# Optimization experiments

Hardware: AMD Instinct MI355X
Metric: run time of the kernel (lower is better)

## Reference

```python
import jax, jax.numpy as jnp
import numpy as np

WIN = 7


def rel_index(win: int) -> jnp.ndarray:
    ys, xs = jnp.meshgrid(jnp.arange(win), jnp.arange(win), indexing='ij')
    coords = jnp.stack([ys.reshape(-1), xs.reshape(-1)], axis=-1)  # (S, 2)
    diff = coords[None, :, :] - coords[:, None, :] + (win - 1)     # (S, S, 2)
    return diff[..., 0] * (2 * win - 1) + diff[..., 1]             # (S, S)


def setup_inputs() -> dict:
    key = jax.random.key(0)
    ks = jax.random.split(key, 5)
    B, WN, S, C, H = 64, 64, WIN * WIN, 192, 6
    X = jax.random.normal(ks[0], (B, WN, S, C), dtype=jnp.float32)
    # torch nn.Linear(emb_dim, 3*emb_dim) -> store as (in, out) for x @ W
    Wqkv = jax.random.normal(ks[1], (C, 3 * C), dtype=jnp.float32) * 0.02
    bqkv = jnp.zeros((3 * C,), dtype=jnp.float32)
    Wo = jax.random.normal(ks[2], (C, C), dtype=jnp.float32) * 0.02
    bo = jnp.zeros((C,), dtype=jnp.float32)
    bias_table = jax.random.normal(ks[3], ((2 * WIN - 1) ** 2, H), dtype=jnp.float32) * 0.02
    return {"X": X, "Wqkv": Wqkv, "bqkv": bqkv, "Wo": Wo, "bo": bo, "bias_table": bias_table}


def reference(X, Wqkv, bqkv, Wo, bo, bias_table):
    B, WN, S, C = X.shape
    H = bias_table.shape[1]
    D = C // H
    scale = D ** -0.5
    # qkv projection: (B, WN, S, 3C) -> (3, B, WN, H, S, D)
    qkv = (X @ Wqkv + bqkv).reshape(B, WN, S, 3, H, D).transpose(3, 0, 1, 4, 2, 5)
    q, k, v = qkv[0], qkv[1], qkv[2]
    attn = jnp.einsum('bwhqd,bwhkd->bwhqk', q, k) * scale  # (B, WN, H, S, S)
    # gathered relative position bias: (S, S, H) -> (H, S, S)
    idx = rel_index(WIN)
    bias = bias_table[idx].transpose(2, 0, 1)
    attn = attn + bias[None, None]
    proba = jax.nn.softmax(attn, axis=-1)  # dropout omitted (eval mode)
    out = jnp.einsum('bwhqk,bwhkd->bwhqd', proba, v)  # (B, WN, H, S, D)
    out = out.transpose(0, 1, 3, 2, 4).reshape(B, WN, S, C)
    return out @ Wo + bo
```

## Files before the change

kernel.cpp:

```cpp
#include <hip/hip_runtime.h>
#include <hip/hip_bf16.h>


typedef __attribute__((ext_vector_type(4))) float f32x4;
typedef __attribute__((ext_vector_type(8))) short bf16x8;
typedef __attribute__((ext_vector_type(4))) unsigned short u16x4;

#define SCALE 0.17677669529663689f
#define MFMA(a, b, acc) __builtin_amdgcn_mfma_f32_16x16x32_bf16(a, b, acc, 0, 0, 0)

__device__ __forceinline__ unsigned short f2bf(float f) {
  union { float f; unsigned int u; } v; v.f = f;
  return (unsigned short)((v.u + 0x7FFFu + ((v.u >> 16) & 1u)) >> 16);
}

__global__ void wprep(const float* __restrict__ Wqkv, const float* __restrict__ Wo,
                      unsigned short* __restrict__ WqkvT, unsigned short* __restrict__ WoT) {
  int i = blockIdx.x * 256 + threadIdx.x;
  if (i < 576 * 192) { int n = i / 192, k = i % 192; WqkvT[i] = f2bf(Wqkv[k * 576 + n]); }
  if (i < 192 * 192) { int n = i / 192, k = i % 192; WoT[i]   = f2bf(Wo[k * 192 + n]); }
}

__global__ __launch_bounds__(512, 4)
void qkv_gemm(const float* __restrict__ X, const unsigned short* __restrict__ WqkvT,
              const float* __restrict__ bqkv, unsigned short* __restrict__ qkv) {
  __shared__ __align__(16) unsigned short Bs[2][64 * 200];
  __shared__ __align__(16) unsigned short scr[8][16 * 72];

  const int tid = threadIdx.x, w8 = tid >> 6, lane = tid & 63;
  const int g = lane >> 4, c = lane & 15;
  const size_t bm = (size_t)blockIdx.x * 128;
  const f32x4 z = {0.f, 0.f, 0.f, 0.f};

  bf16x8 af[6];
  {
    const float* xr = X + (bm + w8 * 16 + c) * 192;
    #pragma unroll
    for (int ks = 0; ks < 6; ++ks) {
      f32x4 lo = *(const f32x4*)(xr + ks * 32 + g * 8);
      f32x4 hi = *(const f32x4*)(xr + ks * 32 + g * 8 + 4);
      bf16x8 a;
      a[0] = (short)f2bf(lo[0]); a[1] = (short)f2bf(lo[1]);
      a[2] = (short)f2bf(lo[2]); a[3] = (short)f2bf(lo[3]);
      a[4] = (short)f2bf(hi[0]); a[5] = (short)f2bf(hi[1]);
      a[6] = (short)f2bf(hi[2]); a[7] = (short)f2bf(hi[3]);
      af[ks] = a;
    }
  }

  uint4 st[3];
  #pragma unroll
  for (int jj = 0; jj < 3; ++jj) {
    int j = tid + jj * 512;
    st[jj] = *(const uint4*)(WqkvT + (j / 24) * 192 + (j % 24) * 8);
  }
  #pragma unroll
  for (int jj = 0; jj < 3; ++jj) {
    int j = tid + jj * 512;
    *(uint4*)(&Bs[0][(j / 24) * 200 + (j % 24) * 8]) = st[jj];
  }
  __syncthreads();

  unsigned short* sw = scr[w8];
  for (int nc = 0; nc < 9; ++nc) {
    const int cur = nc & 1;
    if (nc < 8) {
      #pragma unroll
      for (int jj = 0; jj < 3; ++jj) {
        int j = tid + jj * 512;
        st[jj] = *(const uint4*)(WqkvT + (nc + 1) * 12288 + (j / 24) * 192 + (j % 24) * 8);
      }
    }
    f32x4 acc[4] = {z, z, z, z};
    #pragma unroll
    for (int ks = 0; ks < 6; ++ks) {
      const unsigned short* bp = &Bs[cur][c * 200 + ks * 32 + g * 8];
      #pragma unroll
      for (int nf = 0; nf < 4; ++nf)
        acc[nf] = MFMA(af[ks], *(const bf16x8*)(bp + nf * 16 * 200), acc[nf]);
    }
    #pragma unroll
    for (int nf = 0; nf < 4; ++nf) {
      const float bb = bqkv[nc * 64 + nf * 16 + c];
      #pragma unroll
      for (int r = 0; r < 4; ++r)
        sw[(4 * g + r) * 72 + nf * 16 + c] = f2bf(acc[nf][r] + bb);
    }
    uint4 o0 = *(const uint4*)(sw + c * 72 + g * 8);
    uint4 o1 = *(const uint4*)(sw + c * 72 + 32 + g * 8);
    unsigned short* qp = qkv + (bm + w8 * 16 + c) * 576 + nc * 64;
    *(uint4*)(qp + g * 8)      = o0;
    *(uint4*)(qp + 32 + g * 8) = o1;

    if (nc < 8) {
      #pragma unroll
      for (int jj = 0; jj < 3; ++jj) {
        int j = tid + jj * 512;
        *(uint4*)(&Bs[cur ^ 1][(j / 24) * 200 + (j % 24) * 8]) = st[jj];
      }
    }
    __syncthreads();
  }
}

__global__ __launch_bounds__(512, 4)
void attn_win(unsigned short* __restrict__ qkv, const float* __restrict__ btab) {
  __shared__ __align__(16) unsigned short Ks[64 * 200];
  __shared__ __align__(16) unsigned short Vt[192 * 72];
  __shared__ __align__(16) unsigned short scr[8][1152];
  __shared__ float biasF[1014];

  const int tid = threadIdx.x, w8 = tid >> 6, lane = tid & 63;
  const int g = lane >> 4, c = lane & 15;
  const int mt = w8 & 3, hw = w8 >> 2;
  const size_t tokbase = (size_t)blockIdx.x * 49;
  const f32x4 z = {0.f, 0.f, 0.f, 0.f};

  for (int j = tid; j < 1014; j += 512) biasF[j] = btab[j];
  for (int j = tid; j < 360; j += 512) {
    uint4 zz = {0, 0, 0, 0};
    *(uint4*)(&Ks[(49 + j / 24) * 200 + (j % 24) * 8]) = zz;
  }
  for (int j = tid; j < 2880; j += 512) Vt[(j / 15) * 72 + 49 + j % 15] = 0;
  for (int j = tid; j < 1176; j += 512) {
    int row = j / 24, ch = j % 24;
    *(uint4*)(&Ks[row * 200 + ch * 8]) =
        *(const uint4*)(qkv + (tokbase + row) * 576 + 192 + ch * 8);
  }
  for (int j = tid; j < 1176; j += 512) {
    int row = j / 24, ch = j % 24;
    uint4 v = *(const uint4*)(qkv + (tokbase + row) * 576 + 384 + ch * 8);
    const unsigned short* e = (const unsigned short*)&v;
    #pragma unroll
    for (int k = 0; k < 8; ++k) Vt[(ch * 8 + k) * 72 + row] = e[k];
  }
  __syncthreads();

  const int qbase = mt * 16;
  const int q = qbase + c;
  const bool qvalid = q < 49;
  const int qc = qvalid ? q : 48;
  const int qoff6 = ((6 - qc / 7) * 13 + (6 - qc % 7)) * 6;
  int kb6[16];
  #pragma unroll
  for (int i = 0; i < 16; ++i) {
    int k = (i >> 2) * 16 + g * 4 + (i & 3);
    int kk = k < 49 ? k : 48;
    kb6[i] = ((kk / 7) * 13 + (kk % 7)) * 6;
  }
  unsigned short* Pw = scr[w8];

  for (int hi = 0; hi < 3; ++hi) {
    const int h = hw * 3 + hi;
    const bf16x8 bq = *(const bf16x8*)(qkv + (tokbase + qc) * 576 + h * 32 + g * 8);
    const int cofs = h * 32 + g * 8;
    f32x4 s0 = MFMA(*(const bf16x8*)(Ks + (c) * 200 + cofs), bq, z);
    f32x4 s1 = MFMA(*(const bf16x8*)(Ks + (16 + c) * 200 + cofs), bq, z);
    f32x4 s2 = MFMA(*(const bf16x8*)(Ks + (32 + c) * 200 + cofs), bq, z);
    f32x4 s3 = MFMA(*(const bf16x8*)(Ks + (48 + c) * 200 + cofs), bq, z);

    float p[16];
    float mx = -3e38f;
    #pragma unroll
    for (int i = 0; i < 16; ++i) {
      const int t = i >> 2, r = i & 3;
      const int k = t * 16 + g * 4 + r;
      const float sv = (t == 0) ? s0[r] : (t == 1) ? s1[r] : (t == 2) ? s2[r] : s3[r];
      const float b = biasF[kb6[i] + qoff6 + h];
      const float lg = (qvalid && (k < 49)) ? fmaf(sv, SCALE, b) : -1e30f;
      p[i] = lg;
      mx = fmaxf(mx, lg);
    }
    mx = fmaxf(mx, __shfl_xor(mx, 16));
    mx = fmaxf(mx, __shfl_xor(mx, 32));
    float sum = 0.f;
    #pragma unroll
    for (int i = 0; i < 16; ++i) { p[i] = __expf(p[i] - mx); sum += p[i]; }
    sum += __shfl_xor(sum, 16);
    sum += __shfl_xor(sum, 32);
    const float inv = 1.0f / sum;
    #pragma unroll
    for (int t = 0; t < 4; ++t) {
      u16x4 pk;
      #pragma unroll
      for (int r = 0; r < 4; ++r) pk[r] = f2bf(p[t * 4 + r] * inv);
      *(u16x4*)(Pw + c * 72 + t * 16 + g * 4) = pk;
    }

    f32x4 o0 = z, o1 = z;
    #pragma unroll
    for (int ks = 0; ks < 2; ++ks) {
      const bf16x8 ap = *(const bf16x8*)(Pw + c * 72 + ks * 32 + g * 8);
      const bf16x8 v0 = *(const bf16x8*)(Vt + (h * 32 + c) * 72 + ks * 32 + g * 8);
      const bf16x8 v1 = *(const bf16x8*)(Vt + (h * 32 + 16 + c) * 72 + ks * 32 + g * 8);
      o0 = MFMA(ap, v0, o0);
      o1 = MFMA(ap, v1, o1);
    }
    #pragma unroll
    for (int r = 0; r < 4; ++r) {
      Pw[(4 * g + r) * 72 + c]      = f2bf(o0[r]);
      Pw[(4 * g + r) * 72 + 16 + c] = f2bf(o1[r]);
    }
    uint4 ov = *(const uint4*)(Pw + c * 72 + g * 8);
    if (qvalid)
      *(uint4*)(qkv + (tokbase + q) * 576 + h * 32 + g * 8) = ov;
  }
}

__global__ __launch_bounds__(512, 4)
void out_gemm(const unsigned short* __restrict__ qkv, const unsigned short* __restrict__ WoT,
              const float* __restrict__ bo, float* __restrict__ out) {
  __shared__ __align__(16) unsigned short Ws[192 * 200];

  const int tid = threadIdx.x, w8 = tid >> 6, lane = tid & 63;
  const int g = lane >> 4, c = lane & 15;
  const size_t bm = (size_t)blockIdx.x * 128;
  const f32x4 z = {0.f, 0.f, 0.f, 0.f};

  #pragma unroll
  for (int jj = 0; jj < 9; ++jj) {
    int j = tid + jj * 512;
    *(uint4*)(&Ws[(j / 24) * 200 + (j % 24) * 8]) = *(const uint4*)(WoT + (j / 24) * 192 + (j % 24) * 8);
  }
  __syncthreads();

  bf16x8 af[6];
  #pragma unroll
  for (int ks = 0; ks < 6; ++ks)
    af[ks] = *(const bf16x8*)(qkv + (bm + w8 * 16 + c) * 576 + ks * 32 + g * 8);

  #pragma unroll
  for (int nf = 0; nf < 12; ++nf) {
    const int col = nf * 16 + c;
    const unsigned short* bp = Ws + col * 200;
    f32x4 acc = z;
    #pragma unroll
    for (int ks = 0; ks < 6; ++ks)
      acc = MFMA(af[ks], *(const bf16x8*)(bp + ks * 32 + g * 8), acc);
    const float bb = bo[col];
    #pragma unroll
    for (int r = 0; r < 4; ++r)
      out[(bm + w8 * 16 + 4 * g + r) * 192 + col] = acc[r] + bb;
  }
}

extern "C" void kernel_launch(void* const* d_in, const int* in_sizes, int n_in,
                              void* d_out, int out_size, void* d_ws, size_t ws_size,
                              hipStream_t stream) {
  (void)in_sizes; (void)n_in; (void)out_size; (void)ws_size;
  const float* X    = (const float*)d_in[0];
  const float* Wqkv = (const float*)d_in[1];
  const float* bqkv = (const float*)d_in[2];
  const float* Wo   = (const float*)d_in[3];
  const float* bo   = (const float*)d_in[4];
  const float* btab = (const float*)d_in[5];

  unsigned short* WqkvT = (unsigned short*)d_ws;
  unsigned short* WoT   = WqkvT + 576 * 192;
  unsigned short* qkv   = WoT + 192 * 192;

  wprep<<<432, 256, 0, stream>>>(Wqkv, Wo, WqkvT, WoT);
  qkv_gemm<<<1568, 512, 0, stream>>>(X, WqkvT, bqkv, qkv);
  attn_win<<<4096, 512, 0, stream>>>(qkv, btab);
  out_gemm<<<1568, 512, 0, stream>>>(qkv, WoT, bo, (float*)d_out);
}
```

Measured before the change: 290.7 us.

## Double rows per wave in QKV and output GEMMs; skew V transpose stores

Each wave in the QKV and output projection GEMMs now handles two 16-row M tiles, so every B fragment read from LDS feeds two MFMAs. The block's M tile grows to 256 rows and the grid is halved. This is meant to cut LDS traffic and weight staging per output row, at the cost of more registers and fewer blocks. The V transpose store in the attention kernel is also rotated per channel to reduce LDS bank conflicts.

```diff
diff --git a/kernel.cpp b/kernel.cpp
--- a/kernel.cpp
+++ b/kernel.cpp
@@ -29,12 +29,13 @@
 
   const int tid = threadIdx.x, w8 = tid >> 6, lane = tid & 63;
   const int g = lane >> 4, c = lane & 15;
-  const size_t bm = (size_t)blockIdx.x * 128;
+  const size_t bm = (size_t)blockIdx.x * 256;
   const f32x4 z = {0.f, 0.f, 0.f, 0.f};
 
-  bf16x8 af[6];
-  {
-    const float* xr = X + (bm + w8 * 16 + c) * 192;
+  bf16x8 af0[6], af1[6];
+  #pragma unroll
+  for (int m = 0; m < 2; ++m) {
+    const float* xr = X + (bm + w8 * 32 + m * 16 + c) * 192;
     #pragma unroll
     for (int ks = 0; ks < 6; ++ks) {
       f32x4 lo = *(const f32x4*)(xr + ks * 32 + g * 8);
@@ -44,7 +45,7 @@
       a[2] = (short)f2bf(lo[2]); a[3] = (short)f2bf(lo[3]);
       a[4] = (short)f2bf(hi[0]); a[5] = (short)f2bf(hi[1]);
       a[6] = (short)f2bf(hi[2]); a[7] = (short)f2bf(hi[3]);
-      af[ks] = a;
+      if (m) af1[ks] = a; else af0[ks] = a;
     }
   }
 
@@ -71,26 +72,33 @@
         st[jj] = *(const uint4*)(WqkvT + (nc + 1) * 12288 + (j / 24) * 192 + (j % 24) * 8);
       }
     }
-    f32x4 acc[4] = {z, z, z, z};
+    f32x4 acc0[4] = {z, z, z, z}, acc1[4] = {z, z, z, z};
     #pragma unroll
     for (int ks = 0; ks < 6; ++ks) {
       const unsigned short* bp = &Bs[cur][c * 200 + ks * 32 + g * 8];
       #pragma unroll
-      for (int nf = 0; nf < 4; ++nf)
-        acc[nf] = MFMA(af[ks], *(const bf16x8*)(bp + nf * 16 * 200), acc[nf]);
-    }
-    #pragma unroll
-    for (int nf = 0; nf < 4; ++nf) {
-      const float bb = bqkv[nc * 64 + nf * 16 + c];
-      #pragma unroll
-      for (int r = 0; r < 4; ++r)
-        sw[(4 * g + r) * 72 + nf * 16 + c] = f2bf(acc[nf][r] + bb);
-    }
-    uint4 o0 = *(const uint4*)(sw + c * 72 + g * 8);
-    uint4 o1 = *(const uint4*)(sw + c * 72 + 32 + g * 8);
-    unsigned short* qp = qkv + (bm + w8 * 16 + c) * 576 + nc * 64;
-    *(uint4*)(qp + g * 8)      = o0;
-    *(uint4*)(qp + 32 + g * 8) = o1;
+      for (int nf = 0; nf < 4; ++nf) {
+        bf16x8 bv = *(const bf16x8*)(bp + nf * 16 * 200);
+        acc0[nf] = MFMA(af0[ks], bv, acc0[nf]);
+        acc1[nf] = MFMA(af1[ks], bv, acc1[nf]);
+      }
+    }
+    #pragma unroll
+    for (int m = 0; m < 2; ++m) {
+      #pragma unroll
+      for (int nf = 0; nf < 4; ++nf) {
+        const float bb = bqkv[nc * 64 + nf * 16 + c];
+        const f32x4 a = m ? acc1[nf] : acc0[nf];
+        #pragma unroll
+        for (int r = 0; r < 4; ++r)
+          sw[(4 * g + r) * 72 + nf * 16 + c] = f2bf(a[r] + bb);
+      }
+      uint4 o0 = *(const uint4*)(sw + c * 72 + g * 8);
+      uint4 o1 = *(const uint4*)(sw + c * 72 + 32 + g * 8);
+      unsigned short* qp = qkv + (bm + w8 * 32 + m * 16 + c) * 576 + nc * 64;
+      *(uint4*)(qp + g * 8)      = o0;
+      *(uint4*)(qp + 32 + g * 8) = o1;
+    }
 
     if (nc < 8) {
       #pragma unroll
@@ -132,7 +140,10 @@
     uint4 v = *(const uint4*)(qkv + (tokbase + row) * 576 + 384 + ch * 8);
     const unsigned short* e = (const unsigned short*)&v;
     #pragma unroll
-    for (int k = 0; k < 8; ++k) Vt[(ch * 8 + k) * 72 + row] = e[k];
+    for (int m = 0; m < 8; ++m) {
+      int k = (ch + m) & 7;
+      Vt[(ch * 8 + k) * 72 + row] = e[k];
+    }
   }
   __syncthreads();
 
@@ -214,7 +225,7 @@
 
   const int tid = threadIdx.x, w8 = tid >> 6, lane = tid & 63;
   const int g = lane >> 4, c = lane & 15;
-  const size_t bm = (size_t)blockIdx.x * 128;
+  const size_t bm = (size_t)blockIdx.x * 256;
   const f32x4 z = {0.f, 0.f, 0.f, 0.f};
 
   #pragma unroll
@@ -224,23 +235,30 @@
   }
   __syncthreads();
 
-  bf16x8 af[6];
-  #pragma unroll
-  for (int ks = 0; ks < 6; ++ks)
-    af[ks] = *(const bf16x8*)(qkv + (bm + w8 * 16 + c) * 576 + ks * 32 + g * 8);
+  bf16x8 af0[6], af1[6];
+  #pragma unroll
+  for (int ks = 0; ks < 6; ++ks) {
+    af0[ks] = *(const bf16x8*)(qkv + (bm + w8 * 32 + c) * 576 + ks * 32 + g * 8);
+    af1[ks] = *(const bf16x8*)(qkv + (bm + w8 * 32 + 16 + c) * 576 + ks * 32 + g * 8);
+  }
 
   #pragma unroll
   for (int nf = 0; nf < 12; ++nf) {
     const int col = nf * 16 + c;
     const unsigned short* bp = Ws + col * 200;
-    f32x4 acc = z;
-    #pragma unroll
-    for (int ks = 0; ks < 6; ++ks)
-      acc = MFMA(af[ks], *(const bf16x8*)(bp + ks * 32 + g * 8), acc);
+    f32x4 acc0 = z, acc1 = z;
+    #pragma unroll
+    for (int ks = 0; ks < 6; ++ks) {
+      bf16x8 bv = *(const bf16x8*)(bp + ks * 32 + g * 8);
+      acc0 = MFMA(af0[ks], bv, acc0);
+      acc1 = MFMA(af1[ks], bv, acc1);
+    }
     const float bb = bo[col];
     #pragma unroll
-    for (int r = 0; r < 4; ++r)
-      out[(bm + w8 * 16 + 4 * g + r) * 192 + col] = acc[r] + bb;
+    for (int r = 0; r < 4; ++r) {
+      out[(bm + w8 * 32 + 4 * g + r) * 192 + col]      = acc0[r] + bb;
+      out[(bm + w8 * 32 + 16 + 4 * g + r) * 192 + col] = acc1[r] + bb;
+    }
   }
 }
 
@@ -260,7 +278,7 @@
   unsigned short* qkv   = WoT + 192 * 192;
 
   wprep<<<432, 256, 0, stream>>>(Wqkv, Wo, WqkvT, WoT);
-  qkv_gemm<<<1568, 512, 0, stream>>>(X, WqkvT, bqkv, qkv);
+  qkv_gemm<<<784, 512, 0, stream>>>(X, WqkvT, bqkv, qkv);
   attn_win<<<4096, 512, 0, stream>>>(qkv, btab);
-  out_gemm<<<1568, 512, 0, stream>>>(qkv, WoT, bo, (float*)d_out);
-}
+  out_gemm<<<784, 512, 0, stream>>>(qkv, WoT, bo, (float*)d_out);
+}
```

After: 342.5 us. 17.8% more time.

## Batch QKV output stores in registers and stagger V transpose LDS writes

Applied to the files above, without the earlier changes.

The QKV GEMM loop is fully unrolled, and packed bf16 results for each column chunk are kept in registers instead of being staged and stored to global memory every iteration. The first five chunks are flushed midway through the loop and the last four after it, taking the per-iteration scratch round trip and global stores off the MFMA/prefetch critical path. In the attention kernel, the order of the element writes in the V transpose is rotated per chunk to spread LDS bank accesses. The buffered results add register pressure (20 u16x4 values) under launch_bounds(512,4), which could cause spills or lower occupancy.

```diff
diff --git a/kernel.cpp b/kernel.cpp
--- a/kernel.cpp
+++ b/kernel.cpp
@@ -62,8 +62,28 @@
   __syncthreads();
 
   unsigned short* sw = scr[w8];
+  u16x4 pk[5][4];
+
+  auto flush = [&](int nca, const u16x4* pkc) {
+    #pragma unroll
+    for (int nf = 0; nf < 4; ++nf)
+      #pragma unroll
+      for (int r = 0; r < 4; ++r)
+        sw[(4 * g + r) * 72 + nf * 16 + c] = pkc[nf][r];
+    uint4 o0 = *(const uint4*)(sw + c * 72 + g * 8);
+    uint4 o1 = *(const uint4*)(sw + c * 72 + 32 + g * 8);
+    unsigned short* qp = qkv + (bm + w8 * 16 + c) * 576 + nca * 64;
+    *(uint4*)(qp + g * 8)      = o0;
+    *(uint4*)(qp + 32 + g * 8) = o1;
+  };
+
+  #pragma unroll
   for (int nc = 0; nc < 9; ++nc) {
     const int cur = nc & 1;
+    if (nc == 5) {
+      #pragma unroll
+      for (int f = 0; f < 5; ++f) flush(f, pk[f]);
+    }
     if (nc < 8) {
       #pragma unroll
       for (int jj = 0; jj < 3; ++jj) {
@@ -79,19 +99,15 @@
       for (int nf = 0; nf < 4; ++nf)
         acc[nf] = MFMA(af[ks], *(const bf16x8*)(bp + nf * 16 * 200), acc[nf]);
     }
+    const int slot = nc < 5 ? nc : nc - 5;
     #pragma unroll
     for (int nf = 0; nf < 4; ++nf) {
       const float bb = bqkv[nc * 64 + nf * 16 + c];
-      #pragma unroll
-      for (int r = 0; r < 4; ++r)
-        sw[(4 * g + r) * 72 + nf * 16 + c] = f2bf(acc[nf][r] + bb);
-    }
-    uint4 o0 = *(const uint4*)(sw + c * 72 + g * 8);
-    uint4 o1 = *(const uint4*)(sw + c * 72 + 32 + g * 8);
-    unsigned short* qp = qkv + (bm + w8 * 16 + c) * 576 + nc * 64;
-    *(uint4*)(qp + g * 8)      = o0;
-    *(uint4*)(qp + 32 + g * 8) = o1;
-
+      u16x4 p;
+      #pragma unroll
+      for (int r = 0; r < 4; ++r) p[r] = f2bf(acc[nf][r] + bb);
+      pk[slot][nf] = p;
+    }
     if (nc < 8) {
       #pragma unroll
       for (int jj = 0; jj < 3; ++jj) {
@@ -101,6 +117,8 @@
     }
     __syncthreads();
   }
+  #pragma unroll
+  for (int f = 0; f < 4; ++f) flush(5 + f, pk[f]);
 }
 
 __global__ __launch_bounds__(512, 4)
@@ -132,7 +150,10 @@
     uint4 v = *(const uint4*)(qkv + (tokbase + row) * 576 + 384 + ch * 8);
     const unsigned short* e = (const unsigned short*)&v;
     #pragma unroll
-    for (int k = 0; k < 8; ++k) Vt[(ch * 8 + k) * 72 + row] = e[k];
+    for (int m = 0; m < 8; ++m) {
+      int k = (ch + m) & 7;
+      Vt[(ch * 8 + k) * 72 + row] = e[k];
+    }
   }
   __syncthreads();
 
@@ -181,10 +202,10 @@
     const float inv = 1.0f / sum;
     #pragma unroll
     for (int t = 0; t < 4; ++t) {
-      u16x4 pk;
-      #pragma unroll
-      for (int r = 0; r < 4; ++r) pk[r] = f2bf(p[t * 4 + r] * inv);
-      *(u16x4*)(Pw + c * 72 + t * 16 + g * 4) = pk;
+      u16x4 pkv;
+      #pragma unroll
+      for (int r = 0; r < 4; ++r) pkv[r] = f2bf(p[t * 4 + r] * inv);
+      *(u16x4*)(Pw + c * 72 + t * 16 + g * 4) = pkv;
     }
 
     f32x4 o0 = z, o1 = z;
```

After: 343.2 us. 18.1% more time.

## Fuse output projection into window attention kernel and async-load swizzled QKV weights

Applied to the files above, without the earlier changes.

Merges the attention and output-projection kernels, so each window block keeps its attention output in LDS and multiplies it by Wo in two halves. This removes the global write and re-read of the attention output and one kernel launch. The QKV GEMM now loads weight tiles with global_load_lds into an XOR-swizzled LDS layout, prepared by wprep, instead of staging them through registers. The V transpose store order is also rotated to reduce LDS bank conflicts. In exchange, each window block now reloads the full Wo (two 96-column halves) into LDS, the fused kernel uses more LDS (about 75 KB), which can lower occupancy, and it adds extra barriers.

```diff
diff --git a/kernel.cpp b/kernel.cpp
--- a/kernel.cpp
+++ b/kernel.cpp
@@ -14,18 +14,29 @@
   return (unsigned short)((v.u + 0x7FFFu + ((v.u >> 16) & 1u)) >> 16);
 }
 
+__device__ __forceinline__ void gll16(const unsigned short* src, unsigned short* dst) {
+  __builtin_amdgcn_global_load_lds(
+      (const __attribute__((address_space(1))) unsigned int*)src,
+      (__attribute__((address_space(3))) unsigned int*)dst, 16, 0, 0);
+}
+
 __global__ void wprep(const float* __restrict__ Wqkv, const float* __restrict__ Wo,
-                      unsigned short* __restrict__ WqkvT, unsigned short* __restrict__ WoT) {
+                      unsigned short* __restrict__ WqkvTs, unsigned short* __restrict__ WoT) {
   int i = blockIdx.x * 256 + threadIdx.x;
-  if (i < 576 * 192) { int n = i / 192, k = i % 192; WqkvT[i] = f2bf(Wqkv[k * 576 + n]); }
-  if (i < 192 * 192) { int n = i / 192, k = i % 192; WoT[i]   = f2bf(Wo[k * 192 + n]); }
+  if (i < 576 * 192) {
+    int n = i / 192, k = i % 192;
+    int ch = n >> 6, row = n & 63;
+    int dst = ch * 12288 + row * 192 + (((k >> 3) ^ (row & 7)) << 3) + (k & 7);
+    WqkvTs[dst] = f2bf(Wqkv[k * 576 + n]);
+  }
+  if (i < 192 * 192) { int n = i / 192, k = i % 192; WoT[i] = f2bf(Wo[k * 192 + n]); }
 }
 
 __global__ __launch_bounds__(512, 4)
-void qkv_gemm(const float* __restrict__ X, const unsigned short* __restrict__ WqkvT,
+void qkv_gemm(const float* __restrict__ X, const unsigned short* __restrict__ WqkvTs,
               const float* __restrict__ bqkv, unsigned short* __restrict__ qkv) {
-  __shared__ __align__(16) unsigned short Bs[2][64 * 200];
-  __shared__ __align__(16) unsigned short scr[8][16 * 72];
+  __shared__ __align__(16) unsigned short Bs[2][12288];
+  __shared__ __align__(16) unsigned short scr[8][1152];
 
   const int tid = threadIdx.x, w8 = tid >> 6, lane = tid & 63;
   const int g = lane >> 4, c = lane & 15;
@@ -48,17 +59,9 @@
     }
   }
 
-  uint4 st[3];
-  #pragma unroll
-  for (int jj = 0; jj < 3; ++jj) {
-    int j = tid + jj * 512;
-    st[jj] = *(const uint4*)(WqkvT + (j / 24) * 192 + (j % 24) * 8);
-  }
-  #pragma unroll
-  for (int jj = 0; jj < 3; ++jj) {
-    int j = tid + jj * 512;
-    *(uint4*)(&Bs[0][(j / 24) * 200 + (j % 24) * 8]) = st[jj];
-  }
+  #pragma unroll
+  for (int jj = 0; jj < 3; ++jj)
+    gll16(WqkvTs + (w8 * 3 + jj) * 512 + lane * 8, &Bs[0][(w8 * 3 + jj) * 512]);
   __syncthreads();
 
   unsigned short* sw = scr[w8];
@@ -66,18 +69,19 @@
     const int cur = nc & 1;
     if (nc < 8) {
       #pragma unroll
-      for (int jj = 0; jj < 3; ++jj) {
-        int j = tid + jj * 512;
-        st[jj] = *(const uint4*)(WqkvT + (nc + 1) * 12288 + (j / 24) * 192 + (j % 24) * 8);
+      for (int jj = 0; jj < 3; ++jj)
+        gll16(WqkvTs + (nc + 1) * 12288 + (w8 * 3 + jj) * 512 + lane * 8,
+              &Bs[cur ^ 1][(w8 * 3 + jj) * 512]);
+    }
+    f32x4 acc[4] = {z, z, z, z};
+    #pragma unroll
+    for (int ks = 0; ks < 6; ++ks) {
+      #pragma unroll
+      for (int nf = 0; nf < 4; ++nf) {
+        const bf16x8 bv = *(const bf16x8*)(
+            &Bs[cur][(nf * 16 + c) * 192 + (((ks * 4 + g) ^ (c & 7)) << 3)]);
+        acc[nf] = MFMA(af[ks], bv, acc[nf]);
       }
-    }
-    f32x4 acc[4] = {z, z, z, z};
-    #pragma unroll
-    for (int ks = 0; ks < 6; ++ks) {
-      const unsigned short* bp = &Bs[cur][c * 200 + ks * 32 + g * 8];
-      #pragma unroll
-      for (int nf = 0; nf < 4; ++nf)
-        acc[nf] = MFMA(af[ks], *(const bf16x8*)(bp + nf * 16 * 200), acc[nf]);
     }
     #pragma unroll
     for (int nf = 0; nf < 4; ++nf) {
@@ -91,29 +95,27 @@
     unsigned short* qp = qkv + (bm + w8 * 16 + c) * 576 + nc * 64;
     *(uint4*)(qp + g * 8)      = o0;
     *(uint4*)(qp + 32 + g * 8) = o1;
-
-    if (nc < 8) {
-      #pragma unroll
-      for (int jj = 0; jj < 3; ++jj) {
-        int j = tid + jj * 512;
-        *(uint4*)(&Bs[cur ^ 1][(j / 24) * 200 + (j % 24) * 8]) = st[jj];
-      }
-    }
     __syncthreads();
   }
 }
 
 __global__ __launch_bounds__(512, 4)
-void attn_win(unsigned short* __restrict__ qkv, const float* __restrict__ btab) {
-  __shared__ __align__(16) unsigned short Ks[64 * 200];
-  __shared__ __align__(16) unsigned short Vt[192 * 72];
-  __shared__ __align__(16) unsigned short scr[8][1152];
-  __shared__ float biasF[1014];
+void attn_out(const unsigned short* __restrict__ qkv, const float* __restrict__ btab,
+              const unsigned short* __restrict__ WoT, const float* __restrict__ bo,
+              float* __restrict__ out) {
+  __shared__ __align__(16) unsigned char smem[75776];
+  unsigned short* Ks  = (unsigned short*)smem;
+  unsigned short* Vt  = (unsigned short*)(smem + 25600);
+  unsigned short* scr = (unsigned short*)(smem + 53248);
+  float* biasF        = (float*)(smem + 71680);
+  unsigned short* AOs = (unsigned short*)smem;
+  unsigned short* Wos = (unsigned short*)(smem + 25600);
 
   const int tid = threadIdx.x, w8 = tid >> 6, lane = tid & 63;
   const int g = lane >> 4, c = lane & 15;
   const int mt = w8 & 3, hw = w8 >> 2;
-  const size_t tokbase = (size_t)blockIdx.x * 49;
+  const int wb = blockIdx.x;
+  const size_t tokbase = (size_t)wb * 49;
   const f32x4 z = {0.f, 0.f, 0.f, 0.f};
 
   for (int j = tid; j < 1014; j += 512) biasF[j] = btab[j];
@@ -132,7 +134,10 @@
     uint4 v = *(const uint4*)(qkv + (tokbase + row) * 576 + 384 + ch * 8);
     const unsigned short* e = (const unsigned short*)&v;
     #pragma unroll
-    for (int k = 0; k < 8; ++k) Vt[(ch * 8 + k) * 72 + row] = e[k];
+    for (int m = 0; m < 8; ++m) {
+      int k = (ch + m) & 7;
+      Vt[(ch * 8 + k) * 72 + row] = e[k];
+    }
   }
   __syncthreads();
 
@@ -148,8 +153,10 @@
     int kk = k < 49 ? k : 48;
     kb6[i] = ((kk / 7) * 13 + (kk % 7)) * 6;
   }
-  unsigned short* Pw = scr[w8];
-
+  unsigned short* Pw = scr + w8 * 1152;
+  u16x4 pk0[3], pk1[3];
+
+  #pragma unroll
   for (int hi = 0; hi < 3; ++hi) {
     const int h = hw * 3 + hi;
     const bf16x8 bq = *(const bf16x8*)(qkv + (tokbase + qc) * 576 + h * 32 + g * 8);
@@ -181,10 +188,10 @@
     const float inv = 1.0f / sum;
     #pragma unroll
     for (int t = 0; t < 4; ++t) {
-      u16x4 pk;
-      #pragma unroll
-      for (int r = 0; r < 4; ++r) pk[r] = f2bf(p[t * 4 + r] * inv);
-      *(u16x4*)(Pw + c * 72 + t * 16 + g * 4) = pk;
+      u16x4 pkv;
+      #pragma unroll
+      for (int r = 0; r < 4; ++r) pkv[r] = f2bf(p[t * 4 + r] * inv);
+      *(u16x4*)(Pw + c * 72 + t * 16 + g * 4) = pkv;
     }
 
     f32x4 o0 = z, o1 = z;
@@ -197,50 +204,65 @@
       o1 = MFMA(ap, v1, o1);
     }
     #pragma unroll
+    for (int r = 0; r < 4; ++r) { pk0[hi][r] = f2bf(o0[r]); pk1[hi][r] = f2bf(o1[r]); }
+  }
+  __syncthreads();
+
+  #pragma unroll
+  for (int hi = 0; hi < 3; ++hi) {
+    const int h = hw * 3 + hi;
+    #pragma unroll
     for (int r = 0; r < 4; ++r) {
-      Pw[(4 * g + r) * 72 + c]      = f2bf(o0[r]);
-      Pw[(4 * g + r) * 72 + 16 + c] = f2bf(o1[r]);
-    }
-    uint4 ov = *(const uint4*)(Pw + c * 72 + g * 8);
-    if (qvalid)
-      *(uint4*)(qkv + (tokbase + q) * 576 + h * 32 + g * 8) = ov;
-  }
-}
-
-__global__ __launch_bounds__(512, 4)
-void out_gemm(const unsigned short* __restrict__ qkv, const unsigned short* __restrict__ WoT,
-              const float* __restrict__ bo, float* __restrict__ out) {
-  __shared__ __align__(16) unsigned short Ws[192 * 200];
-
-  const int tid = threadIdx.x, w8 = tid >> 6, lane = tid & 63;
-  const int g = lane >> 4, c = lane & 15;
-  const size_t bm = (size_t)blockIdx.x * 128;
-  const f32x4 z = {0.f, 0.f, 0.f, 0.f};
-
-  #pragma unroll
-  for (int jj = 0; jj < 9; ++jj) {
-    int j = tid + jj * 512;
-    *(uint4*)(&Ws[(j / 24) * 200 + (j % 24) * 8]) = *(const uint4*)(WoT + (j / 24) * 192 + (j % 24) * 8);
-  }
-  __syncthreads();
-
-  bf16x8 af[6];
+      AOs[(mt * 16 + 4 * g + r) * 200 + h * 32 + c]      = pk0[hi][r];
+      AOs[(mt * 16 + 4 * g + r) * 200 + h * 32 + 16 + c] = pk1[hi][r];
+    }
+  }
+  for (int j = tid; j < 2304; j += 512)
+    *(uint4*)(&Wos[(j / 24) * 200 + (j % 24) * 8]) =
+        *(const uint4*)(WoT + (j / 24) * 192 + (j % 24) * 8);
+  __syncthreads();
+
+  bf16x8 af2[6];
   #pragma unroll
   for (int ks = 0; ks < 6; ++ks)
-    af[ks] = *(const bf16x8*)(qkv + (bm + w8 * 16 + c) * 576 + ks * 32 + g * 8);
-
-  #pragma unroll
-  for (int nf = 0; nf < 12; ++nf) {
-    const int col = nf * 16 + c;
-    const unsigned short* bp = Ws + col * 200;
+    af2[ks] = *(const bf16x8*)(AOs + (mt * 16 + c) * 200 + ks * 32 + g * 8);
+  float* og = out + (size_t)wb * 9408;
+
+  #pragma unroll
+  for (int ct = 0; ct < 3; ++ct) {
+    const int col = hw * 48 + ct * 16 + c;
+    const unsigned short* bp = Wos + col * 200;
     f32x4 acc = z;
     #pragma unroll
     for (int ks = 0; ks < 6; ++ks)
-      acc = MFMA(af[ks], *(const bf16x8*)(bp + ks * 32 + g * 8), acc);
+      acc = MFMA(af2[ks], *(const bf16x8*)(bp + ks * 32 + g * 8), acc);
     const float bb = bo[col];
     #pragma unroll
-    for (int r = 0; r < 4; ++r)
-      out[(bm + w8 * 16 + 4 * g + r) * 192 + col] = acc[r] + bb;
+    for (int r = 0; r < 4; ++r) {
+      const int row = mt * 16 + 4 * g + r;
+      if (row < 49) og[row * 192 + col] = acc[r] + bb;
+    }
+  }
+  __syncthreads();
+  for (int j = tid; j < 2304; j += 512)
+    *(uint4*)(&Wos[(j / 24) * 200 + (j % 24) * 8]) =
+        *(const uint4*)(WoT + (96 + j / 24) * 192 + (j % 24) * 8);
+  __syncthreads();
+
+  #pragma unroll
+  for (int ct = 0; ct < 3; ++ct) {
+    const int col = 96 + hw * 48 + ct * 16 + c;
+    const unsigned short* bp = Wos + (col - 96) * 200;
+    f32x4 acc = z;
+    #pragma unroll
+    for (int ks = 0; ks < 6; ++ks)
+      acc = MFMA(af2[ks], *(const bf16x8*)(bp + ks * 32 + g * 8), acc);
+    const float bb = bo[col];
+    #pragma unroll
+    for (int r = 0; r < 4; ++r) {
+      const int row = mt * 16 + 4 * g + r;
+      if (row < 49) og[row * 192 + col] = acc[r] + bb;
+    }
   }
 }
 
@@ -255,12 +277,11 @@
   const float* bo   = (const float*)d_in[4];
   const float* btab = (const float*)d_in[5];
 
-  unsigned short* WqkvT = (unsigned short*)d_ws;
-  unsigned short* WoT   = WqkvT + 576 * 192;
-  unsigned short* qkv   = WoT + 192 * 192;
-
-  wprep<<<432, 256, 0, stream>>>(Wqkv, Wo, WqkvT, WoT);
-  qkv_gemm<<<1568, 512, 0, stream>>>(X, WqkvT, bqkv, qkv);
-  attn_win<<<4096, 512, 0, stream>>>(qkv, btab);
-  out_gemm<<<1568, 512, 0, stream>>>(qkv, WoT, bo, (float*)d_out);
-}
+  unsigned short* WqkvTs = (unsigned short*)d_ws;
+  unsigned short* WoT    = WqkvTs + 576 * 192;
+  unsigned short* qkv    = WoT + 192 * 192;
+
+  wprep<<<432, 256, 0, stream>>>(Wqkv, Wo, WqkvTs, WoT);
+  qkv_gemm<<<1568, 512, 0, stream>>>(X, WqkvTs, bqkv, qkv);
+  attn_out<<<4096, 512, 0, stream>>>(qkv, btab, WoT, bo, (float*)d_out);
+}
```

Result: slower. 322.5 us (+10.9%).
